# Kernel optimization log

Measured on AMD Instinct MI355X. Metric: run time of the kernel, lower is better.

The kernel has to match this reference:

```python
import jax, jax.numpy as jnp
import numpy as np

B, C, H, W = 64, 3, 64, 64
F = 96          # base_filters
K = 8           # n_mixtures
h, w = H // 2, W // 2
C0 = 2 * C      # channels of each checkerboard half
SECTIONS = [C0, C0, C0 * K, C0 * K, C0 * K]
SPLITS = [int(s) for s in np.cumsum(SECTIONS)[:-1]]
EPS = 1e-6


def conv2d(x, wgt, b):
    y = jax.lax.conv_general_dilated(x, wgt, (1, 1), 'SAME',
                                     dimension_numbers=('NCHW', 'OIHW', 'NCHW'))
    return y + b[None, :, None, None]


def layer_norm(x, g, b, eps=1e-5):
    # nn.LayerNorm(mid_shape): normalize over (C,H,W) per sample
    mu = jnp.mean(x, axis=(1, 2, 3), keepdims=True)
    var = jnp.var(x, axis=(1, 2, 3), keepdims=True)
    return (x - mu) / jnp.sqrt(var + eps) * g[None] + b[None]


def checker_split(z, odd=False):
    Bz, Cz, Hz, Wz = z.shape
    z = z.reshape(Bz, Cz, Hz // 2, 2, Wz // 2, 2)
    p00 = z[:, :, :, 0, :, 0]; p01 = z[:, :, :, 0, :, 1]
    p10 = z[:, :, :, 1, :, 0]; p11 = z[:, :, :, 1, :, 1]
    z0 = jnp.concatenate([p00, p11], axis=1)  # even checkerboard
    z1 = jnp.concatenate([p01, p10], axis=1)  # odd checkerboard
    if odd:
        z0, z1 = z1, z0
    return z0, z1


def checker_merge(z0, z1, odd=False):
    if odd:
        z0, z1 = z1, z0
    Cz = z0.shape[1] // 2
    p00, p11 = z0[:, :Cz], z0[:, Cz:]
    p01, p10 = z1[:, :Cz], z1[:, Cz:]
    Bz, _, hz, wz = p00.shape
    zi = jnp.stack([jnp.stack([p00, p01], axis=-1),
                    jnp.stack([p10, p11], axis=-1)], axis=-2)  # (B,C,h,w,2i,2j)
    z = zi.transpose(0, 1, 2, 4, 3, 5).reshape(Bz, Cz, 2 * hz, 2 * wz)
    return z


def gated_attn(x, qkv_w, qkv_b, proj_w, proj_b):
    Bx, Fx, hx, wx = x.shape
    xf = x.reshape(Bx, Fx, hx * wx).transpose(0, 2, 1)  # (B, L, F)
    qkv = xf @ qkv_w.T + qkv_b
    q, k, v = jnp.split(qkv, 3, axis=-1)
    scores = jnp.einsum('bqf,bkf->bqk', q, k) / jnp.sqrt(jnp.float32(Fx))
    attn = jax.nn.softmax(scores, axis=-1)
    o = jnp.einsum('bqk,bkf->bqf', attn, v)
    g = o @ proj_w.T + proj_b
    ga, gb = jnp.split(g, 2, axis=-1)
    out = xf + ga * jax.nn.sigmoid(gb)  # gated residual
    return out.transpose(0, 2, 1).reshape(Bx, Fx, hx, wx)


def conditioner(z1, conv1_w, conv1_b, gconv_w, gconv_b, ln1_g, ln1_b,
                qkv_w, qkv_b, proj_w, proj_b, ln2_g, ln2_b, conv2_w, conv2_b):
    x = conv2d(z1, conv1_w, conv1_b)
    g = conv2d(x, gconv_w, gconv_b)
    ga, gb = jnp.split(g, 2, axis=1)
    x = x + ga * jax.nn.sigmoid(gb)          # GatedConv2d
    x = layer_norm(x, ln1_g, ln1_b)
    x = gated_attn(x, qkv_w, qkv_b, proj_w, proj_b)
    x = layer_norm(x, ln2_g, ln2_b)
    return conv2d(x, conv2_w, conv2_b)


def _forward(z, log_df_dz, conv1_w, conv1_b, gconv_w, gconv_b, ln1_g, ln1_b,
             qkv_w, qkv_b, proj_w, proj_b, ln2_g, ln2_b, conv2_w, conv2_b,
             a_log_scale, a_bias):
    z0, z1 = checker_split(z)
    params = conditioner(z1, conv1_w, conv1_b, gconv_w, gconv_b, ln1_g, ln1_b,
                         qkv_w, qkv_b, proj_w, proj_b, ln2_g, ln2_b, conv2_w, conv2_b)
    a, b, logpi, mu, s = jnp.split(params, SPLITS, axis=1)
    a = jnp.tanh(a) * a_log_scale + a_bias
    Bz = z0.shape[0]
    logpi = jax.nn.log_softmax(logpi.reshape(Bz, K, C0, h, w), axis=1)
    mu = mu.reshape(Bz, K, C0, h, w)
    s = s.reshape(Bz, K, C0, h, w)
    # mixture-of-logistics CDF
    u = (z0[:, None] - mu) * jnp.exp(-s)
    x = jnp.sum(jnp.exp(logpi) * jax.nn.sigmoid(u), axis=1)
    log_pdf = jax.scipy.special.logsumexp(
        logpi - s + jax.nn.log_sigmoid(u) + jax.nn.log_sigmoid(-u), axis=1)
    log_df_dz = log_df_dz + jnp.sum(log_pdf.reshape(Bz, -1), axis=1)
    # logit transform
    x = jnp.clip(x, EPS, 1.0 - EPS)
    z0n = jnp.log(x) - jnp.log1p(-x)
    log_df_dz = log_df_dz + jnp.sum((-jnp.log(x) - jnp.log1p(-x)).reshape(Bz, -1), axis=1)
    # affine rescale
    z0n = z0n * jnp.exp(a) + b
    log_df_dz = log_df_dz + jnp.sum(a.reshape(Bz, -1), axis=1)
    return checker_merge(z0n, z1), log_df_dz


def setup_inputs() -> dict:
    key = jax.random.key(0)
    ks = jax.random.split(key, 10)
    sc = 0.05
    return dict(
        z=jax.random.normal(ks[0], (B, C, H, W), jnp.float32),
        log_df_dz=jnp.zeros((B,), jnp.float32),
        conv1_w=sc * jax.random.normal(ks[1], (F, C0, 3, 3), jnp.float32),
        conv1_b=jnp.zeros((F,), jnp.float32),
        gconv_w=sc * jax.random.normal(ks[2], (2 * F, F, 3, 3), jnp.float32),
        gconv_b=jnp.zeros((2 * F,), jnp.float32),
        ln1_g=jnp.ones((F, h, w), jnp.float32),
        ln1_b=jnp.zeros((F, h, w), jnp.float32),
        qkv_w=sc * jax.random.normal(ks[3], (3 * F, F), jnp.float32),
        qkv_b=jnp.zeros((3 * F,), jnp.float32),
        proj_w=sc * jax.random.normal(ks[4], (2 * F, F), jnp.float32),
        proj_b=jnp.zeros((2 * F,), jnp.float32),
        ln2_g=jnp.ones((F, h, w), jnp.float32),
        ln2_b=jnp.zeros((F, h, w), jnp.float32),
        conv2_w=sc * jax.random.normal(ks[5], (sum(SECTIONS), F, 3, 3), jnp.float32),
        conv2_b=jnp.zeros((sum(SECTIONS),), jnp.float32),
        a_log_scale=0.01 * jax.random.normal(ks[6], (1,), jnp.float32),
        a_bias=0.01 * jax.random.normal(ks[7], (1,), jnp.float32),
    )


def reference(z, log_df_dz, conv1_w, conv1_b, gconv_w, gconv_b, ln1_g, ln1_b,
              qkv_w, qkv_b, proj_w, proj_b, ln2_g, ln2_b, conv2_w, conv2_b,
              a_log_scale, a_bias):
    return _forward(z, log_df_dz, conv1_w, conv1_b, gconv_w, gconv_b, ln1_g, ln1_b,
                    qkv_w, qkv_b, proj_w, proj_b, ln2_g, ln2_b, conv2_w, conv2_b,
                    a_log_scale, a_bias)
```

## Files before the change

kernel.cpp:

```cpp
#include <hip/hip_runtime.h>
#include <cstdint>
#include <cstddef>


typedef unsigned short u16;
typedef __attribute__((ext_vector_type(8))) short short8;
typedef __attribute__((ext_vector_type(4))) float f32x4;
typedef __attribute__((ext_vector_type(4))) unsigned int u32x4;

__device__ __forceinline__ float sigm(float x){ return 1.0f/(1.0f+__expf(-x)); }

__device__ __forceinline__ u16 f2bf(float f){
    unsigned int u = __float_as_uint(f);
    u += 0x7fffu + ((u >> 16) & 1u);
    return (u16)(u >> 16);
}
__device__ __forceinline__ float bf2f(u16 v){
    unsigned int u = ((unsigned int)v) << 16;
    return __uint_as_float(u);
}

__device__ __forceinline__ float ex2(float x){
    float r; asm("v_exp_f32 %0, %1" : "=v"(r) : "v"(x)); return r;
}
__device__ __forceinline__ unsigned cvtpk(float lo, float hi){
    unsigned r; asm("v_cvt_pk_bf16_f32 %0, %1, %2" : "=v"(r) : "v"(lo), "v"(hi)); return r;
}
__device__ __forceinline__ void plswap32(unsigned &a, unsigned &b){
    asm("v_permlane32_swap_b32 %0, %1" : "+v"(a), "+v"(b));
}
__device__ __forceinline__ void plswap16(unsigned &a, unsigned &b){
    asm("v_permlane16_swap_b32 %0, %1" : "+v"(a), "+v"(b));
}

#define SOFTPACK(S, LACC, PA) do { \
    unsigned pk_[4][2]; \
    _Pragma("unroll") \
    for (int t=0;t<4;++t){ \
        float e0 = ex2(S[t][0]); \
        float e1 = ex2(S[t][1]); \
        float e2 = ex2(S[t][2]); \
        float e3 = ex2(S[t][3]); \
        LACC += (e0+e1)+(e2+e3); \
        pk_[t][0] = cvtpk(e0,e1); \
        pk_[t][1] = cvtpk(e2,e3); \
    } \
    _Pragma("unroll") \
    for (int kk=0;kk<2;++kk){ \
        unsigned a0 = pk_[2*kk][0], b0 = pk_[2*kk+1][0]; \
        unsigned a1 = pk_[2*kk][1], b1 = pk_[2*kk+1][1]; \
        plswap32(a0,b0); plswap16(a0,b0); \
        plswap32(a1,b1); plswap16(a1,b1); \
        u32x4 dw_; dw_[0]=a0; dw_[1]=a1; dw_[2]=b0; dw_[3]=b1; \
        PA[kk] = __builtin_bit_cast(short8, dw_); \
    } \
} while(0)

__global__ __launch_bounds__(256) void k_prep(
    const float* __restrict__ z, const float* __restrict__ c1w, const float* __restrict__ c1b,
    const float* __restrict__ gw, const float* __restrict__ c2w,
    const float* __restrict__ qkvw, const float* __restrict__ pw,
    const float* __restrict__ ln1g, const float* __restrict__ ln1b,
    const float* __restrict__ ln2g, const float* __restrict__ ln2b,
    const float* __restrict__ logdf,
    u16* __restrict__ x1b,
    u16* __restrict__ Wg, u16* __restrict__ W2,
    u16* __restrict__ Wqkv, u16* __restrict__ Wproj,
    float* __restrict__ gt1, float* __restrict__ bt1,
    float* __restrict__ gt2, float* __restrict__ bt2,
    float* __restrict__ outlog)
{
    int blk = blockIdx.x;
    int tid = threadIdx.x;
    __shared__ float tin[6][6][34];
    __shared__ __align__(16) u16 Wc[96][72];
    __shared__ __align__(16) u16 imc[128][72];

    if (blk < 512){
        int b  = blk >> 3;
        int pg = blk & 7;
        int r0 = pg*4;
        for (int e = tid; e < 96*72; e += 256){
            int oc = e/72, k = e%72;
            Wc[oc][k] = (k < 54) ? f2bf(c1w[oc*54 + k]) : (u16)0;
        }
        for (int idx = tid; idx < 6*6*34; idx += 256){
            int c = idx/204, rem = idx%204;
            int rr = rem/34, q = rem%34;
            int ii = r0 - 1 + rr, jj = q - 1;
            float v = 0.f;
            if ((unsigned)ii < 32u && (unsigned)jj < 32u){
                if (c < 3) v = z[((b*3+c)*64 + 2*ii)*64 + (2*jj+1)];
                else       v = z[((b*3+(c-3))*64 + (2*ii+1))*64 + 2*jj];
            }
            tin[c][rr][q] = v;
        }
        __syncthreads();
        for (int e = tid; e < 128*72; e += 256){
            int px = e/72, k = e%72;
            float v = 0.f;
            if (k < 54){
                int c = k/9, rr = (k%9)/3, dcc = k%3;
                v = tin[c][(px>>5)+rr][(px&31)+dcc];
            }
            imc[px][k] = f2bf(v);
        }
        __syncthreads();

        int w = tid >> 6, lane = tid & 63;
        int cc = lane & 15, gg = lane >> 4;
        f32x4 acc[2][6];
        #pragma unroll
        for (int u=0;u<2;++u)
            #pragma unroll
            for (int t=0;t<6;++t) acc[u][t] = (f32x4){0.f,0.f,0.f,0.f};

        #pragma unroll
        for (int ks=0; ks<2; ++ks){
            short8 a0 = *reinterpret_cast<const short8*>(&imc[w*32 + cc     ][ks*32 + 8*gg]);
            short8 a1 = *reinterpret_cast<const short8*>(&imc[w*32 + 16 + cc][ks*32 + 8*gg]);
            #pragma unroll
            for (int t=0; t<6; ++t){
                short8 bb = *reinterpret_cast<const short8*>(&Wc[t*16+cc][ks*32 + 8*gg]);
                acc[0][t] = __builtin_amdgcn_mfma_f32_16x16x32_bf16(a0, bb, acc[0][t], 0,0,0);
                acc[1][t] = __builtin_amdgcn_mfma_f32_16x16x32_bf16(a1, bb, acc[1][t], 0,0,0);
            }
        }

        #pragma unroll
        for (int u=0;u<2;++u){
            int p0 = pg*128 + w*32 + u*16 + gg*4;
            #pragma unroll
            for (int t=0;t<6;++t){
                int oc = t*16+cc;
                float bv = c1b[oc];
                #pragma unroll
                for (int r=0;r<4;++r)
                    x1b[((size_t)(b*1024) + p0 + r)*96 + oc] = f2bf(acc[u][t][r] + bv);
            }
        }
    } else if (blk < 1160){
        int idx = (blk-512)*256 + tid;
        int tap = idx / (192*96);
        int rem = idx - tap*192*96;
        int ocp = rem / 96, ic = rem % 96;
        int obk = ocp/96, r = ocp%96, isB = r/48, i = r%48;
        int oc = obk*48 + i + isB*96;
        Wg[idx] = f2bf(gw[(size_t)(oc*96+ic)*9 + tap]);
    } else if (blk < 1700){
        int idx = (blk-1160)*256 + tid;
        int tap = idx / (160*96);
        int rem = idx - tap*160*96;
        int oc = rem / 96, ic = rem % 96;
        W2[idx] = (oc < 156) ? f2bf(c2w[(size_t)(oc*96+ic)*9 + tap]) : (u16)0;
    } else if (blk < 1808){
        int idx = (blk-1700)*256 + tid;
        Wqkv[idx] = f2bf(qkvw[idx]);
    } else if (blk < 1880){
        int idx = (blk-1808)*256 + tid;
        int ocp = idx / 96, ic = idx % 96;
        int obk = ocp/96, r = ocp%96, isB = r/48, i = r%48;
        int oc = obk*48 + i + isB*96;
        Wproj[idx] = f2bf(pw[(size_t)oc*96 + ic]);
    } else if (blk < 2264){
        int idx = (blk-1880)*256 + tid;
        int c = idx >> 10, p = idx & 1023;
        gt1[p*96 + c] = ln1g[idx];
    } else if (blk < 2648){
        int idx = (blk-2264)*256 + tid;
        int c = idx >> 10, p = idx & 1023;
        bt1[p*96 + c] = ln1b[idx];
    } else if (blk < 3032){
        int idx = (blk-2648)*256 + tid;
        int c = idx >> 10, p = idx & 1023;
        gt2[p*96 + c] = ln2g[idx];
    } else if (blk < 3416){
        int idx = (blk-3032)*256 + tid;
        int c = idx >> 10, p = idx & 1023;
        bt2[p*96 + c] = ln2b[idx];
    } else {
        if (tid < 64) outlog[tid] = logdf[tid];
    }
}

__global__ __launch_bounds__(256,4) void k_gconv(const u16* __restrict__ Xpb,
    const u16* __restrict__ Wt, const float* __restrict__ bias,
    u16* __restrict__ outb, float* __restrict__ partials)
{
    int blk  = blockIdx.x;
    int obk  = blk & 1;
    int pblk = (blk >> 1) & 7;
    int b    = blk >> 4;
    int tid  = threadIdx.x;
    int w = tid >> 6, lane = tid & 63;
    int cc = lane & 15, gg = lane >> 4;

    __shared__ __align__(16) u16 Ws[96][104];
    __shared__ float red[8];

    f32x4 acc[2][6];
    #pragma unroll
    for (int u=0;u<2;++u)
        #pragma unroll
        for (int t=0;t<6;++t) acc[u][t] = (f32x4){0.f,0.f,0.f,0.f};

    int base = pblk*128 + w*32;
    int ia = base >> 5;
    const u16* xb = Xpb + (size_t)b*1024*96;
    const u16* wbase = Wt + (size_t)obk*96*96;

    short8 wreg[5];
    #pragma unroll
    for (int i=0;i<5;++i){
        int c = tid + 256*i;
        if (c < 1152){
            int oc=c/12, ico=(c%12)*8;
            wreg[i] = *reinterpret_cast<const short8*>(wbase + oc*96 + ico);
        }
    }

    for (int tap=0; tap<9; ++tap){
        int dr = tap/3 - 1, dc = tap%3 - 1;
        __syncthreads();
        #pragma unroll
        for (int i=0;i<5;++i){
            int c = tid + 256*i;
            if (c < 1152){
                int oc=c/12, ico=(c%12)*8;
                *reinterpret_cast<short8*>(&Ws[oc][ico]) = wreg[i];
            }
        }
        if (tap < 8){
            const u16* wn = wbase + (size_t)(tap+1)*192*96;
            #pragma unroll
            for (int i=0;i<5;++i){
                int c = tid + 256*i;
                if (c < 1152){
                    int oc=c/12, ico=(c%12)*8;
                    wreg[i] = *reinterpret_cast<const short8*>(wn + oc*96 + ico);
                }
            }
        }
        __syncthreads();

        int ii = ia + dr;
        int jj0 = cc + dc, jj1 = cc + 16 + dc;
        bool rv = ((unsigned)ii < 32u);
        bool v0 = rv && ((unsigned)jj0 < 32u);
        bool v1 = rv && ((unsigned)jj1 < 32u);
        const u16* ar0 = xb + (ptrdiff_t)(ii*32 + jj0)*96 + 8*gg;
        const u16* ar1 = xb + (ptrdiff_t)(ii*32 + jj1)*96 + 8*gg;

        #pragma unroll
        for (int ks=0; ks<3; ++ks){
            short8 a0 = {0,0,0,0,0,0,0,0};
            short8 a1 = {0,0,0,0,0,0,0,0};
            if (v0) a0 = *reinterpret_cast<const short8*>(ar0 + ks*32);
            if (v1) a1 = *reinterpret_cast<const short8*>(ar1 + ks*32);
            #pragma unroll
            for (int t=0; t<6; ++t){
                short8 bb = *reinterpret_cast<const short8*>(&Ws[t*16+cc][ks*32+8*gg]);
                acc[0][t] = __builtin_amdgcn_mfma_f32_16x16x32_bf16(a0, bb, acc[0][t], 0,0,0);
                acc[1][t] = __builtin_amdgcn_mfma_f32_16x16x32_bf16(a1, bb, acc[1][t], 0,0,0);
            }
        }
    }

    float s = 0.f, ssq = 0.f;
    #pragma unroll
    for (int u=0;u<2;++u){
        int p0 = base + u*16 + gg*4;
        #pragma unroll
        for (int t=0;t<3;++t){
            int ocA = obk*48 + t*16+cc;
            float ba = bias[ocA], bbv = bias[ocA+96];
            #pragma unroll
            for (int r=0;r<4;++r){
                float res = bf2f(Xpb[((size_t)b*1024 + p0+r)*96 + ocA]);
                float va = acc[u][t][r]   + ba;
                float vb = acc[u][t+3][r] + bbv;
                float v = res + va*sigm(vb);
                outb[((size_t)b*1024 + p0+r)*96 + ocA] = f2bf(v);
                s += v; ssq += v*v;
            }
        }
    }
    #pragma unroll
    for (int o=32;o>0;o>>=1){ s += __shfl_down(s,o,64); ssq += __shfl_down(ssq,o,64); }
    if (lane==0){ red[w]=s; red[4+w]=ssq; }
    __syncthreads();
    if (tid==0){
        int slot = b*16 + pblk*2 + obk;
        partials[slot*2+0] = red[0]+red[1]+red[2]+red[3];
        partials[slot*2+1] = red[4]+red[5]+red[6]+red[7];
    }
}

__global__ __launch_bounds__(256) void k_lne(const u16* __restrict__ xb,
    const float* __restrict__ gt, const float* __restrict__ bt,
    const float* __restrict__ partials, u16* __restrict__ out)
{
    int b = blockIdx.x / 48, rem = blockIdx.x % 48;
    float s=0.f, ss=0.f;
    #pragma unroll
    for (int i=0;i<16;++i){ s += partials[(b*16+i)*2]; ss += partials[(b*16+i)*2+1]; }
    float mu = s/98304.f;
    float r = rsqrtf(ss/98304.f - mu*mu + 1e-5f);

    int e8 = rem*256 + threadIdx.x;
    size_t base = (size_t)b*98304 + (size_t)e8*8;
    short8 x8 = *reinterpret_cast<const short8*>(xb + base);
    const float* gp = gt + e8*8;
    const float* bp = bt + e8*8;
    short8 o8;
    #pragma unroll
    for (int i=0;i<8;++i)
        o8[i] = (short)f2bf((bf2f((u16)x8[i]) - mu)*r*gp[i] + bp[i]);
    *reinterpret_cast<short8*>(out + base) = o8;
}

__global__ __launch_bounds__(256,4) void k_conv2m(const u16* __restrict__ Xpb,
    const u16* __restrict__ Wt, const float* __restrict__ bias,
    u16* __restrict__ out)
{
    int blk  = blockIdx.x;
    int obk  = blk & 1;
    int pblk = (blk >> 1) & 7;
    int b    = blk >> 4;
    int tid  = threadIdx.x;
    int w = tid >> 6, lane = tid & 63;
    int cc = lane & 15, gg = lane >> 4;

    __shared__ __align__(16) u16 Ws[80][104];

    f32x4 acc[2][5];
    #pragma unroll
    for (int u=0;u<2;++u)
        #pragma unroll
        for (int t=0;t<5;++t) acc[u][t] = (f32x4){0.f,0.f,0.f,0.f};

    int base = pblk*128 + w*32;
    int ia = base >> 5;
    const u16* xb = Xpb + (size_t)b*1024*96;
    const u16* wbase = Wt + (size_t)obk*80*96;

    short8 wreg[4];
    #pragma unroll
    for (int i=0;i<4;++i){
        int c = tid + 256*i;
        if (c < 960){
            int oc=c/12, ico=(c%12)*8;
            wreg[i] = *reinterpret_cast<const short8*>(wbase + oc*96 + ico);
        }
    }

    for (int tap=0; tap<9; ++tap){
        int dr = tap/3 - 1, dc = tap%3 - 1;
        __syncthreads();
        #pragma unroll
        for (int i=0;i<4;++i){
            int c = tid + 256*i;
            if (c < 960){
                int oc=c/12, ico=(c%12)*8;
                *reinterpret_cast<short8*>(&Ws[oc][ico]) = wreg[i];
            }
        }
        if (tap < 8){
            const u16* wn = wbase + (size_t)(tap+1)*160*96;
            #pragma unroll
            for (int i=0;i<4;++i){
                int c = tid + 256*i;
                if (c < 960){
                    int oc=c/12, ico=(c%12)*8;
                    wreg[i] = *reinterpret_cast<const short8*>(wn + oc*96 + ico);
                }
            }
        }
        __syncthreads();

        int ii = ia + dr;
        int jj0 = cc + dc, jj1 = cc + 16 + dc;
        bool rv = ((unsigned)ii < 32u);
        bool v0 = rv && ((unsigned)jj0 < 32u);
        bool v1 = rv && ((unsigned)jj1 < 32u);
        const u16* ar0 = xb + (ptrdiff_t)(ii*32 + jj0)*96 + 8*gg;
        const u16* ar1 = xb + (ptrdiff_t)(ii*32 + jj1)*96 + 8*gg;

        #pragma unroll
        for (int ks=0; ks<3; ++ks){
            short8 a0 = {0,0,0,0,0,0,0,0};
            short8 a1 = {0,0,0,0,0,0,0,0};
            if (v0) a0 = *reinterpret_cast<const short8*>(ar0 + ks*32);
            if (v1) a1 = *reinterpret_cast<const short8*>(ar1 + ks*32);
            #pragma unroll
            for (int t=0; t<5; ++t){
                short8 bb = *reinterpret_cast<const short8*>(&Ws[t*16+cc][ks*32+8*gg]);
                acc[0][t] = __builtin_amdgcn_mfma_f32_16x16x32_bf16(a0, bb, acc[0][t], 0,0,0);
                acc[1][t] = __builtin_amdgcn_mfma_f32_16x16x32_bf16(a1, bb, acc[1][t], 0,0,0);
            }
        }
    }

    #pragma unroll
    for (int u=0;u<2;++u){
        int p0 = base + u*16 + gg*4;
        #pragma unroll
        for (int t=0;t<5;++t){
            int oc = obk*80 + t*16+cc;
            if (oc < 156){
                float bv = bias[oc];
                u16* op = out + ((size_t)b*156 + oc)*1024 + p0;
                #pragma unroll
                for (int r=0;r<4;++r) op[r] = f2bf(acc[u][t][r] + bv);
            }
        }
    }
}

__global__ __launch_bounds__(256,4) void k_qkvm(const u16* __restrict__ Xpb,
    const u16* __restrict__ Wt, const float* __restrict__ bias,
    u16* __restrict__ Qb, u16* __restrict__ Kf, u16* __restrict__ Vf)
{
    int blk  = blockIdx.x;
    int obk  = blk & 1;
    int pblk = (blk >> 1) & 7;
    int b    = blk >> 4;
    int tid  = threadIdx.x;
    int w = tid >> 6, lane = tid & 63;
    int cc = lane & 15, gg = lane >> 4;
    const float scale = 0.14724445f;

    __shared__ __align__(16) u16 Ws[144][104];
    {
        const u16* wp = Wt + (size_t)obk*144*96;
        for (int c = tid; c < 144*12; c += 256){
            int oc = c/12, ico = (c%12)*8;
            *reinterpret_cast<short8*>(&Ws[oc][ico]) =
                *reinterpret_cast<const short8*>(wp + oc*96 + ico);
        }
    }

    f32x4 acc[2][9];
    #pragma unroll
    for (int u=0;u<2;++u)
        #pragma unroll
        for (int t=0;t<9;++t) acc[u][t] = (f32x4){0.f,0.f,0.f,0.f};

    int base = pblk*128 + w*32;
    const u16* xb = Xpb + ((size_t)b*1024 + base)*96;
    __syncthreads();

    #pragma unroll
    for (int ks=0; ks<3; ++ks){
        short8 a0 = *reinterpret_cast<const short8*>(xb + (size_t)cc*96      + ks*32 + 8*gg);
        short8 a1 = *reinterpret_cast<const short8*>(xb + (size_t)(cc+16)*96 + ks*32 + 8*gg);
        #pragma unroll
        for (int t=0; t<9; ++t){
            short8 bb = *reinterpret_cast<const short8*>(&Ws[t*16+cc][ks*32+8*gg]);
            acc[0][t] = __builtin_amdgcn_mfma_f32_16x16x32_bf16(a0, bb, acc[0][t], 0,0,0);
            acc[1][t] = __builtin_amdgcn_mfma_f32_16x16x32_bf16(a1, bb, acc[1][t], 0,0,0);
        }
    }

    #pragma unroll
    for (int u=0;u<2;++u){
        int p0 = base + u*16 + gg*4;
        #pragma unroll
        for (int t=0;t<9;++t){
            int n = obk*144 + t*16+cc;
            float bv = bias[n];
            #pragma unroll
            for (int r=0;r<4;++r){
                int p = p0 + r;
                float av = acc[u][t][r] + bv;
                if (n < 96){
                    Qb[((size_t)(b*1024+p))*96 + n] = f2bf(av*scale);
                } else if (n < 192){
                    int f = n-96;
                    int jt = p>>6, t16 = (p>>4)&3, ccs = p&15;
                    int ks = f>>5, ggs = (f>>3)&3, j = f&7;
                    Kf[(size_t)(b*16+jt)*6144 + (size_t)(((t16*3+ks)*4+ggs)*16+ccs)*8 + j] = f2bf(av);
                } else {
                    int f = n-192;
                    int jt = p>>6, kl = p&63;
                    int kk = kl>>5, ggs = (kl>>3)&3, j = kl&7;
                    int ft = f>>4, ccs = f&15;
                    Vf[(size_t)(b*16+jt)*6144 + (size_t)(((ft*2+kk)*4+ggs)*16+ccs)*8 + j] = f2bf(av);
                }
            }
        }
    }
}

__global__ __launch_bounds__(256,2) void k_attn(const u16* __restrict__ Qb,
    const u16* __restrict__ Kf, const u16* __restrict__ Vf, u16* __restrict__ Ob)
{
    int qt = blockIdx.x >> 6;
    int b  = blockIdx.x & 63;
    int tid = threadIdx.x;
    int w  = tid >> 6;
    int lane = tid & 63;
    int cc = lane & 15;
    int gg = lane >> 4;

    __shared__ __align__(16) u16 Ks[2][6144];
    __shared__ __align__(16) u16 Vs[2][6144];

    int q0 = qt*128 + w*32;

    short8 qf[2][3];
    {
        const u16* qr0 = Qb + ((size_t)(b*1024 + q0 + cc))*96;
        #pragma unroll
        for (int ks=0; ks<3; ++ks){
            qf[0][ks] = *reinterpret_cast<const short8*>(qr0 + ks*32 + 8*gg);
            qf[1][ks] = *reinterpret_cast<const short8*>(qr0 + (size_t)16*96 + ks*32 + 8*gg);
        }
    }

    f32x4 Oacc[2][6];
    #pragma unroll
    for (int u=0;u<2;++u)
        #pragma unroll
        for (int ft=0; ft<6; ++ft) Oacc[u][ft] = (f32x4){0.f,0.f,0.f,0.f};
    float l_acc[2] = {0.f, 0.f};

    const u16* Kb0 = Kf + (size_t)(b*16)*6144;
    const u16* Vb0 = Vf + (size_t)(b*16)*6144;

    short8 kreg[3], vreg[3];
    #pragma unroll
    for (int i=0;i<3;++i){
        int s8 = (tid + 256*i)*8;
        kreg[i] = *reinterpret_cast<const short8*>(Kb0 + s8);
        vreg[i] = *reinterpret_cast<const short8*>(Vb0 + s8);
    }
    #pragma unroll
    for (int i=0;i<3;++i){
        int s8 = (tid + 256*i)*8;
        *reinterpret_cast<short8*>(Ks[0] + s8) = kreg[i];
        *reinterpret_cast<short8*>(Vs[0] + s8) = vreg[i];
    }
    #pragma unroll
    for (int i=0;i<3;++i){
        int s8 = (tid + 256*i)*8;
        kreg[i] = *reinterpret_cast<const short8*>(Kb0 + 6144 + s8);
        vreg[i] = *reinterpret_cast<const short8*>(Vb0 + 6144 + s8);
    }

    for (int jt=0; jt<16; ++jt){
        __syncthreads();
        if (jt < 15){
            int nb = (jt+1)&1;
            #pragma unroll
            for (int i=0;i<3;++i){
                int s8 = (tid + 256*i)*8;
                *reinterpret_cast<short8*>(Ks[nb] + s8) = kreg[i];
                *reinterpret_cast<short8*>(Vs[nb] + s8) = vreg[i];
            }
        }
        if (jt < 14){
            const u16* kn = Kb0 + (size_t)(jt+2)*6144;
            const u16* vn = Vb0 + (size_t)(jt+2)*6144;
            #pragma unroll
            for (int i=0;i<3;++i){
                int s8 = (tid + 256*i)*8;
                kreg[i] = *reinterpret_cast<const short8*>(kn + s8);
                vreg[i] = *reinterpret_cast<const short8*>(vn + s8);
            }
        }

        const u16* Kc = Ks[jt&1];
        const u16* Vc = Vs[jt&1];

        f32x4 S0[4], S1[4];
        #pragma unroll
        for (int t=0;t<4;++t){ S0[t] = (f32x4){0.f,0.f,0.f,0.f}; S1[t] = (f32x4){0.f,0.f,0.f,0.f}; }

        __builtin_amdgcn_s_setprio(1);
        #pragma unroll
        for (int ks=0; ks<3; ++ks){
            #pragma unroll
            for (int t=0; t<4; ++t){
                short8 kb = *reinterpret_cast<const short8*>(Kc + ((t*3+ks)*64 + lane)*8);
                S0[t] = __builtin_amdgcn_mfma_f32_16x16x32_bf16(kb, qf[0][ks], S0[t], 0,0,0);
                S1[t] = __builtin_amdgcn_mfma_f32_16x16x32_bf16(kb, qf[1][ks], S1[t], 0,0,0);
            }
        }
        __builtin_amdgcn_s_setprio(0);

        short8 pa0[2], pa1[2];
        SOFTPACK(S0, l_acc[0], pa0);
        SOFTPACK(S1, l_acc[1], pa1);

        __builtin_amdgcn_s_setprio(1);
        #pragma unroll
        for (int kk=0; kk<2; ++kk){
            #pragma unroll
            for (int ft=0; ft<6; ++ft){
                short8 vb = *reinterpret_cast<const short8*>(Vc + ((ft*2+kk)*64 + lane)*8);
                Oacc[0][ft] = __builtin_amdgcn_mfma_f32_16x16x32_bf16(pa0[kk], vb, Oacc[0][ft], 0,0,0);
                Oacc[1][ft] = __builtin_amdgcn_mfma_f32_16x16x32_bf16(pa1[kk], vb, Oacc[1][ft], 0,0,0);
            }
        }
        __builtin_amdgcn_s_setprio(0);
    }

    #pragma unroll
    for (int u=0;u<2;++u){
        float lv = l_acc[u];
        lv += __shfl_xor(lv, 16, 64);
        lv += __shfl_xor(lv, 32, 64);
        float linv[4];
        #pragma unroll
        for (int r=0;r<4;++r) linv[r] = 1.0f / __shfl(lv, 4*gg + r, 64);
        #pragma unroll
        for (int ft=0; ft<6; ++ft)
            #pragma unroll
            for (int r=0; r<4; ++r)
                Ob[((size_t)(b*1024 + q0 + u*16 + 4*gg + r))*96 + ft*16 + cc]
                    = f2bf(Oacc[u][ft][r]*linv[r]);
    }
}

__global__ __launch_bounds__(256,4) void k_projm(const u16* __restrict__ Opb,
    const u16* __restrict__ Wt, const float* __restrict__ bias,
    const u16* __restrict__ xlnb, u16* __restrict__ outb, float* __restrict__ partials)
{
    int blk  = blockIdx.x;
    int obk  = blk & 1;
    int pblk = (blk >> 1) & 7;
    int b    = blk >> 4;
    int tid  = threadIdx.x;
    int w = tid >> 6, lane = tid & 63;
    int cc = lane & 15, gg = lane >> 4;

    __shared__ __align__(16) u16 Ws[96][104];
    __shared__ float red[8];
    {
        const u16* wp = Wt + (size_t)obk*96*96;
        for (int c = tid; c < 96*12; c += 256){
            int oc = c/12, ico = (c%12)*8;
            *reinterpret_cast<short8*>(&Ws[oc][ico]) =
                *reinterpret_cast<const short8*>(wp + oc*96 + ico);
        }
    }

    f32x4 acc[2][6];
    #pragma unroll
    for (int u=0;u<2;++u)
        #pragma unroll
        for (int t=0;t<6;++t) acc[u][t] = (f32x4){0.f,0.f,0.f,0.f};

    int base = pblk*128 + w*32;
    const u16* xb = Opb + ((size_t)b*1024 + base)*96;
    __syncthreads();

    #pragma unroll
    for (int ks=0; ks<3; ++ks){
        short8 a0 = *reinterpret_cast<const short8*>(xb + (size_t)cc*96      + ks*32 + 8*gg);
        short8 a1 = *reinterpret_cast<const short8*>(xb + (size_t)(cc+16)*96 + ks*32 + 8*gg);
        #pragma unroll
        for (int t=0; t<6; ++t){
            short8 bb = *reinterpret_cast<const short8*>(&Ws[t*16+cc][ks*32+8*gg]);
            acc[0][t] = __builtin_amdgcn_mfma_f32_16x16x32_bf16(a0, bb, acc[0][t], 0,0,0);
            acc[1][t] = __builtin_amdgcn_mfma_f32_16x16x32_bf16(a1, bb, acc[1][t], 0,0,0);
        }
    }

    const u16* resb = xlnb + (size_t)b*1024*96;
    float s = 0.f, ssq = 0.f;
    #pragma unroll
    for (int u=0;u<2;++u){
        int p0 = base + u*16 + gg*4;
        #pragma unroll
        for (int t=0;t<3;++t){
            int ocA = obk*48 + t*16+cc;
            float ba = bias[ocA], bbv = bias[ocA+96];
            #pragma unroll
            for (int r=0;r<4;++r){
                float ga = acc[u][t][r]   + ba;
                float gb = acc[u][t+3][r] + bbv;
                float res = bf2f(resb[(size_t)(p0+r)*96 + ocA]);
                float v = res + ga * sigm(gb);
                outb[((size_t)b*1024 + p0+r)*96 + ocA] = f2bf(v);
                s += v; ssq += v*v;
            }
        }
    }
    #pragma unroll
    for (int o=32;o>0;o>>=1){ s += __shfl_down(s,o,64); ssq += __shfl_down(ssq,o,64); }
    if (lane==0){ red[w]=s; red[4+w]=ssq; }
    __syncthreads();
    if (tid==0){
        int slot = b*16 + pblk*2 + obk;
        partials[slot*2+0] = red[0]+red[1]+red[2]+red[3];
        partials[slot*2+1] = red[4]+red[5]+red[6]+red[7];
    }
}

__global__ __launch_bounds__(256) void k_mix(const float* __restrict__ z,
    const u16* __restrict__ params, const float* __restrict__ a_ls_p,
    const float* __restrict__ a_b_p, float* __restrict__ out_z, float* __restrict__ out_log)
{
    int b = blockIdx.x / 24;
    int rem = blockIdx.x % 24;
    int c0 = rem / 4;
    int pix = (rem & 3)*256 + threadIdx.x;
    int i = pix >> 5, j = pix & 31;
    float als = a_ls_p[0], abv = a_b_p[0];
    const u16* pb = params + (size_t)b*156*1024;
    float logacc = 0.f;

    if (c0 < 3){
        int idx01 = ((b*3+c0)*64 + 2*i)*64 + 2*j+1;
        int idx10 = ((b*3+c0)*64 + 2*i+1)*64 + 2*j;
        out_z[idx01] = z[idx01];
        out_z[idx10] = z[idx10];
    }

    {
        float z0v = (c0<3) ? z[((b*3+c0)*64 + 2*i)*64 + 2*j]
                           : z[((b*3+(c0-3))*64 + 2*i+1)*64 + 2*j+1];
        float a_raw = bf2f(pb[(c0)*1024 + pix]);
        float bco   = bf2f(pb[(6+c0)*1024 + pix]);
        float lp[8], mu[8], sv[8];
        float m1 = -1e30f;
        #pragma unroll
        for (int k=0;k<8;++k){
            lp[k] = bf2f(pb[(12 + k*6 + c0)*1024 + pix]);
            mu[k] = bf2f(pb[(60 + k*6 + c0)*1024 + pix]);
            sv[k] = bf2f(pb[(108 + k*6 + c0)*1024 + pix]);
            m1 = fmaxf(m1, lp[k]);
        }
        float se = 0.f;
        #pragma unroll
        for (int k=0;k<8;++k) se += __expf(lp[k]-m1);
        float lse = m1 + __logf(se);
        float xm = 0.f, mt = -1e30f;
        float t[8];
        #pragma unroll
        for (int k=0;k<8;++k){
            float lpn = lp[k] - lse;
            float u = (z0v - mu[k]) * __expf(-sv[k]);
            float au = fabsf(u);
            xm += __expf(lpn) * (1.f/(1.f+__expf(-u)));
            float lss = -(au + 2.f*log1pf(__expf(-au)));
            float tk = lpn - sv[k] + lss;
            t[k] = tk; mt = fmaxf(mt, tk);
        }
        float se2 = 0.f;
        #pragma unroll
        for (int k=0;k<8;++k) se2 += __expf(t[k]-mt);
        logacc += mt + __logf(se2);
        xm = fminf(fmaxf(xm, 1e-6f), 1.f-1e-6f);
        float lx = __logf(xm), l1x = log1pf(-xm);
        logacc += -lx - l1x;
        float aa = tanhf(a_raw)*als + abv;
        float z0n = (lx - l1x)*__expf(aa) + bco;
        logacc += aa;
        int oidx = (c0<3) ? ((b*3+c0)*64 + 2*i)*64 + 2*j
                          : ((b*3+(c0-3))*64 + 2*i+1)*64 + 2*j+1;
        out_z[oidx] = z0n;
    }

    #pragma unroll
    for (int o=32;o>0;o>>=1) logacc += __shfl_down(logacc, o, 64);
    __shared__ float part[4];
    if ((threadIdx.x&63)==0) part[threadIdx.x>>6] = logacc;
    __syncthreads();
    if (threadIdx.x==0){
        atomicAdd(out_log + b, part[0]+part[1]+part[2]+part[3]);
    }
}

extern "C" void kernel_launch(void* const* d_in, const int* in_sizes, int n_in,
                              void* d_out, int out_size, void* d_ws, size_t ws_size,
                              hipStream_t stream)
{
    const float* z     = (const float*)d_in[0];
    const float* logdf = (const float*)d_in[1];
    const float* c1w   = (const float*)d_in[2];
    const float* c1b   = (const float*)d_in[3];
    const float* gw    = (const float*)d_in[4];
    const float* gcb   = (const float*)d_in[5];
    const float* ln1g  = (const float*)d_in[6];
    const float* ln1b  = (const float*)d_in[7];
    const float* qkvw  = (const float*)d_in[8];
    const float* qkvb  = (const float*)d_in[9];
    const float* pw    = (const float*)d_in[10];
    const float* pbb   = (const float*)d_in[11];
    const float* ln2g  = (const float*)d_in[12];
    const float* ln2b  = (const float*)d_in[13];
    const float* c2w   = (const float*)d_in[14];
    const float* c2b   = (const float*)d_in[15];
    const float* als   = (const float*)d_in[16];
    const float* ab    = (const float*)d_in[17];

    float* out_z   = (float*)d_out;
    float* out_log = out_z + 786432;

    float* ws     = (float*)d_ws;
    u16*   x1b    = (u16*)(ws + 0);
    u16*   xg_b   = (u16*)(ws + 3145728);
    u16*   xlnb   = (u16*)(ws + 6291456);
    u16*   Vf     = (u16*)(ws + 9437184);
    u16*   Ob     = (u16*)(ws + 12582912);
    u16*   x2b    = (u16*)(ws + 15728640);
    u16*   Qb     = x1b;
    u16*   Kf     = xg_b;
    u16*   xln2b  = xlnb;
    u16*   params = (u16*)(ws + 9437184);
    const size_t T = 19660800;
    float* gt1    = ws + T;
    float* bt1    = ws + T + 98304;
    float* gt2    = ws + T + 196608;
    float* bt2    = ws + T + 294912;
    float* part1  = ws + T + 393216;
    float* part2  = ws + T + 395264;
    u16*   Wg     = (u16*)(ws + T + 397568);
    u16*   W2     = (u16*)(ws + T + 480512);
    u16*   Wqkv   = (u16*)(ws + T + 549632);
    u16*   Wproj  = (u16*)(ws + T + 563456);

    k_prep   <<<3417, 256, 0, stream>>>(z, c1w, c1b, gw, c2w, qkvw, pw,
                                        ln1g, ln1b, ln2g, ln2b, logdf,
                                        x1b, Wg, W2, Wqkv, Wproj,
                                        gt1, bt1, gt2, bt2, out_log);
    k_gconv  <<<1024, 256, 0, stream>>>(x1b, Wg, gcb, xg_b, part1);
    k_lne    <<<3072, 256, 0, stream>>>(xg_b, gt1, bt1, part1, xlnb);
    k_qkvm   <<<1024, 256, 0, stream>>>(xlnb, Wqkv, qkvb, Qb, Kf, Vf);
    k_attn   <<<512, 256, 0, stream>>>(Qb, Kf, Vf, Ob);
    k_projm  <<<1024, 256, 0, stream>>>(Ob, Wproj, pbb, xlnb, x2b, part2);
    k_lne    <<<3072, 256, 0, stream>>>(x2b, gt2, bt2, part2, xln2b);
    k_conv2m <<<1024, 256, 0, stream>>>(xln2b, W2, c2b, params);
    k_mix    <<<1536, 256, 0, stream>>>(z, params, als, ab, out_z, out_log);
}
```

Before: 270.5 us.

## Fuse first LayerNorm into QKV and proj GEMMs; DMA pre-swizzled weights to LDS

The first LayerNorm kernel is dropped. Its normalization is now applied on the fly when loading A fragments in the QKV GEMM and again in the proj residual epilogue, so one full activation write and read pass goes away. Weight matrices are reordered in the prep kernel into MFMA fragment order, which lets conv, QKV, proj and attention K/V tiles be copied straight into LDS with global_load_lds. That replaces the register-staged copies and adds double buffering in the conv kernels. In exchange, the LN math is recomputed per fragment and the gamma/beta fp32 tables are read twice, and the workspace buffers are reassigned.

```diff
diff --git a/kernel.cpp b/kernel.cpp
--- a/kernel.cpp
+++ b/kernel.cpp
@@ -18,6 +18,13 @@
 __device__ __forceinline__ float bf2f(u16 v){
     unsigned int u = ((unsigned int)v) << 16;
     return __uint_as_float(u);
+}
+
+__device__ __forceinline__ void dma16(const u16* g, u16* l){
+    __builtin_amdgcn_global_load_lds(
+        (const __attribute__((address_space(1))) void*)g,
+        (__attribute__((address_space(3))) void*)l,
+        16, 0, 0);
 }
 
 __device__ __forceinline__ float ex2(float x){
@@ -56,6 +63,22 @@
     } \
 } while(0)
 
+__device__ __forceinline__ short8 ln_frag(const u16* __restrict__ xg,
+    const float* __restrict__ gt, const float* __restrict__ bt,
+    int p, int c0, float mu, float rr)
+{
+    short8 x8 = *reinterpret_cast<const short8*>(xg + (size_t)p*96 + c0);
+    const float* gp = gt + (size_t)p*96 + c0;
+    const float* bp = bt + (size_t)p*96 + c0;
+    short8 o;
+    #pragma unroll
+    for (int j=0;j<8;++j){
+        float ag = rr*gp[j];
+        o[j] = (short)f2bf(bf2f((u16)x8[j])*ag + (bp[j] - mu*ag));
+    }
+    return o;
+}
+
 __global__ __launch_bounds__(256) void k_prep(
     const float* __restrict__ z, const float* __restrict__ c1w, const float* __restrict__ c1b,
     const float* __restrict__ gw, const float* __restrict__ c2w,
@@ -141,26 +164,57 @@
         }
     } else if (blk < 1160){
         int idx = (blk-512)*256 + tid;
-        int tap = idx / (192*96);
-        int rem = idx - tap*192*96;
-        int ocp = rem / 96, ic = rem % 96;
-        int obk = ocp/96, r = ocp%96, isB = r/48, i = r%48;
-        int oc = obk*48 + i + isB*96;
+        int j = idx & 7;
+        int lane = (idx >> 3) & 63;
+        int fo = idx >> 9;
+        int frag = fo % 18;
+        int tob = fo / 18;
+        int obk = tob & 1, tap = tob >> 1;
+        int t = frag/3, ks = frag%3;
+        int cc = lane & 15, gg = lane >> 4;
+        int ocp = obk*96 + t*16 + cc;
+        int r2 = ocp%96, isB = r2/48, i2 = r2%48;
+        int oc = (ocp/96)*48 + i2 + isB*96;
+        int ic = ks*32 + 8*gg + j;
         Wg[idx] = f2bf(gw[(size_t)(oc*96+ic)*9 + tap]);
     } else if (blk < 1700){
         int idx = (blk-1160)*256 + tid;
-        int tap = idx / (160*96);
-        int rem = idx - tap*160*96;
-        int oc = rem / 96, ic = rem % 96;
+        int j = idx & 7;
+        int lane = (idx >> 3) & 63;
+        int fo = idx >> 9;
+        int frag = fo % 15;
+        int tob = fo / 15;
+        int obk = tob & 1, tap = tob >> 1;
+        int t = frag/3, ks = frag%3;
+        int cc = lane & 15, gg = lane >> 4;
+        int oc = obk*80 + t*16 + cc;
+        int ic = ks*32 + 8*gg + j;
         W2[idx] = (oc < 156) ? f2bf(c2w[(size_t)(oc*96+ic)*9 + tap]) : (u16)0;
     } else if (blk < 1808){
         int idx = (blk-1700)*256 + tid;
-        Wqkv[idx] = f2bf(qkvw[idx]);
+        int j = idx & 7;
+        int lane = (idx >> 3) & 63;
+        int fo = idx >> 9;
+        int frag = fo % 27;
+        int obk = fo / 27;
+        int t = frag/3, ks = frag%3;
+        int cc = lane & 15, gg = lane >> 4;
+        int n = obk*144 + t*16 + cc;
+        int ic = ks*32 + 8*gg + j;
+        Wqkv[idx] = f2bf(qkvw[(size_t)n*96 + ic]);
     } else if (blk < 1880){
         int idx = (blk-1808)*256 + tid;
-        int ocp = idx / 96, ic = idx % 96;
-        int obk = ocp/96, r = ocp%96, isB = r/48, i = r%48;
-        int oc = obk*48 + i + isB*96;
+        int j = idx & 7;
+        int lane = (idx >> 3) & 63;
+        int fo = idx >> 9;
+        int frag = fo % 18;
+        int obk = fo / 18;
+        int t = frag/3, ks = frag%3;
+        int cc = lane & 15, gg = lane >> 4;
+        int ocp = obk*96 + t*16 + cc;
+        int r2 = ocp%96, isB = r2/48, i2 = r2%48;
+        int oc = obk*48 + i2 + isB*96;
+        int ic = ks*32 + 8*gg + j;
         Wproj[idx] = f2bf(pw[(size_t)oc*96 + ic]);
     } else if (blk < 2264){
         int idx = (blk-1880)*256 + tid;
@@ -195,7 +249,7 @@
     int w = tid >> 6, lane = tid & 63;
     int cc = lane & 15, gg = lane >> 4;
 
-    __shared__ __align__(16) u16 Ws[96][104];
+    __shared__ __align__(16) u16 Ws[2][9216];
     __shared__ float red[8];
 
     f32x4 acc[2][6];
@@ -207,41 +261,29 @@
     int base = pblk*128 + w*32;
     int ia = base >> 5;
     const u16* xb = Xpb + (size_t)b*1024*96;
-    const u16* wbase = Wt + (size_t)obk*96*96;
-
-    short8 wreg[5];
-    #pragma unroll
-    for (int i=0;i<5;++i){
-        int c = tid + 256*i;
-        if (c < 1152){
-            int oc=c/12, ico=(c%12)*8;
-            wreg[i] = *reinterpret_cast<const short8*>(wbase + oc*96 + ico);
-        }
-    }
-
-    for (int tap=0; tap<9; ++tap){
-        int dr = tap/3 - 1, dc = tap%3 - 1;
-        __syncthreads();
+
+    {
+        const u16* src = Wt + (size_t)obk*9216;
         #pragma unroll
         for (int i=0;i<5;++i){
             int c = tid + 256*i;
-            if (c < 1152){
-                int oc=c/12, ico=(c%12)*8;
-                *reinterpret_cast<short8*>(&Ws[oc][ico]) = wreg[i];
-            }
-        }
+            if (c < 1152) dma16(src + (size_t)c*8, Ws[0] + (size_t)(w*64+256*i)*8);
+        }
+    }
+
+    for (int tap=0; tap<9; ++tap){
+        __syncthreads();
         if (tap < 8){
-            const u16* wn = wbase + (size_t)(tap+1)*192*96;
+            const u16* src = Wt + (size_t)((tap+1)*2 + obk)*9216;
+            int nb = (tap+1)&1;
             #pragma unroll
             for (int i=0;i<5;++i){
                 int c = tid + 256*i;
-                if (c < 1152){
-                    int oc=c/12, ico=(c%12)*8;
-                    wreg[i] = *reinterpret_cast<const short8*>(wn + oc*96 + ico);
-                }
-            }
-        }
-        __syncthreads();
+                if (c < 1152) dma16(src + (size_t)c*8, Ws[nb] + (size_t)(w*64+256*i)*8);
+            }
+        }
+        const u16* Wc = Ws[tap&1];
+        int dr = tap/3 - 1, dc = tap%3 - 1;
 
         int ii = ia + dr;
         int jj0 = cc + dc, jj1 = cc + 16 + dc;
@@ -259,7 +301,7 @@
             if (v1) a1 = *reinterpret_cast<const short8*>(ar1 + ks*32);
             #pragma unroll
             for (int t=0; t<6; ++t){
-                short8 bb = *reinterpret_cast<const short8*>(&Ws[t*16+cc][ks*32+8*gg]);
+                short8 bb = *reinterpret_cast<const short8*>(Wc + ((size_t)(t*3+ks)*64 + lane)*8);
                 acc[0][t] = __builtin_amdgcn_mfma_f32_16x16x32_bf16(a0, bb, acc[0][t], 0,0,0);
                 acc[1][t] = __builtin_amdgcn_mfma_f32_16x16x32_bf16(a1, bb, acc[1][t], 0,0,0);
             }
@@ -331,7 +373,7 @@
     int w = tid >> 6, lane = tid & 63;
     int cc = lane & 15, gg = lane >> 4;
 
-    __shared__ __align__(16) u16 Ws[80][104];
+    __shared__ __align__(16) u16 Ws[2][7680];
 
     f32x4 acc[2][5];
     #pragma unroll
@@ -342,41 +384,29 @@
     int base = pblk*128 + w*32;
     int ia = base >> 5;
     const u16* xb = Xpb + (size_t)b*1024*96;
-    const u16* wbase = Wt + (size_t)obk*80*96;
-
-    short8 wreg[4];
-    #pragma unroll
-    for (int i=0;i<4;++i){
-        int c = tid + 256*i;
-        if (c < 960){
-            int oc=c/12, ico=(c%12)*8;
-            wreg[i] = *reinterpret_cast<const short8*>(wbase + oc*96 + ico);
-        }
-    }
-
-    for (int tap=0; tap<9; ++tap){
-        int dr = tap/3 - 1, dc = tap%3 - 1;
-        __syncthreads();
+
+    {
+        const u16* src = Wt + (size_t)obk*7680;
         #pragma unroll
         for (int i=0;i<4;++i){
             int c = tid + 256*i;
-            if (c < 960){
-                int oc=c/12, ico=(c%12)*8;
-                *reinterpret_cast<short8*>(&Ws[oc][ico]) = wreg[i];
-            }
-        }
+            if (c < 960) dma16(src + (size_t)c*8, Ws[0] + (size_t)(w*64+256*i)*8);
+        }
+    }
+
+    for (int tap=0; tap<9; ++tap){
+        __syncthreads();
         if (tap < 8){
-            const u16* wn = wbase + (size_t)(tap+1)*160*96;
+            const u16* src = Wt + (size_t)((tap+1)*2 + obk)*7680;
+            int nb = (tap+1)&1;
             #pragma unroll
             for (int i=0;i<4;++i){
                 int c = tid + 256*i;
-                if (c < 960){
-                    int oc=c/12, ico=(c%12)*8;
-                    wreg[i] = *reinterpret_cast<const short8*>(wn + oc*96 + ico);
-                }
-            }
-        }
-        __syncthreads();
+                if (c < 960) dma16(src + (size_t)c*8, Ws[nb] + (size_t)(w*64+256*i)*8);
+            }
+        }
+        const u16* Wc = Ws[tap&1];
+        int dr = tap/3 - 1, dc = tap%3 - 1;
 
         int ii = ia + dr;
         int jj0 = cc + dc, jj1 = cc + 16 + dc;
@@ -394,7 +424,7 @@
             if (v1) a1 = *reinterpret_cast<const short8*>(ar1 + ks*32);
             #pragma unroll
             for (int t=0; t<5; ++t){
-                short8 bb = *reinterpret_cast<const short8*>(&Ws[t*16+cc][ks*32+8*gg]);
+                short8 bb = *reinterpret_cast<const short8*>(Wc + ((size_t)(t*3+ks)*64 + lane)*8);
                 acc[0][t] = __builtin_amdgcn_mfma_f32_16x16x32_bf16(a0, bb, acc[0][t], 0,0,0);
                 acc[1][t] = __builtin_amdgcn_mfma_f32_16x16x32_bf16(a1, bb, acc[1][t], 0,0,0);
             }
@@ -417,7 +447,9 @@
     }
 }
 
-__global__ __launch_bounds__(256,4) void k_qkvm(const u16* __restrict__ Xpb,
+__global__ __launch_bounds__(256,4) void k_qkvm(const u16* __restrict__ Xg,
+    const float* __restrict__ gt, const float* __restrict__ bt,
+    const float* __restrict__ part,
     const u16* __restrict__ Wt, const float* __restrict__ bias,
     u16* __restrict__ Qb, u16* __restrict__ Kf, u16* __restrict__ Vf)
 {
@@ -430,15 +462,21 @@
     int cc = lane & 15, gg = lane >> 4;
     const float scale = 0.14724445f;
 
-    __shared__ __align__(16) u16 Ws[144][104];
+    __shared__ __align__(16) u16 Ws[13824];
     {
-        const u16* wp = Wt + (size_t)obk*144*96;
-        for (int c = tid; c < 144*12; c += 256){
-            int oc = c/12, ico = (c%12)*8;
-            *reinterpret_cast<short8*>(&Ws[oc][ico]) =
-                *reinterpret_cast<const short8*>(wp + oc*96 + ico);
-        }
-    }
+        const u16* src = Wt + (size_t)obk*13824;
+        #pragma unroll
+        for (int i=0;i<7;++i){
+            int c = tid + 256*i;
+            if (c < 1728) dma16(src + (size_t)c*8, Ws + (size_t)(w*64+256*i)*8);
+        }
+    }
+
+    float sS=0.f, sQ=0.f;
+    #pragma unroll
+    for (int i=0;i<16;++i){ sS += part[(b*16+i)*2]; sQ += part[(b*16+i)*2+1]; }
+    float mu = sS/98304.f;
+    float rr = rsqrtf(sQ/98304.f - mu*mu + 1e-5f);
 
     f32x4 acc[2][9];
     #pragma unroll
@@ -447,16 +485,17 @@
         for (int t=0;t<9;++t) acc[u][t] = (f32x4){0.f,0.f,0.f,0.f};
 
     int base = pblk*128 + w*32;
-    const u16* xb = Xpb + ((size_t)b*1024 + base)*96;
+    const u16* xg = Xg + (size_t)b*1024*96;
     __syncthreads();
 
     #pragma unroll
     for (int ks=0; ks<3; ++ks){
-        short8 a0 = *reinterpret_cast<const short8*>(xb + (size_t)cc*96      + ks*32 + 8*gg);
-        short8 a1 = *reinterpret_cast<const short8*>(xb + (size_t)(cc+16)*96 + ks*32 + 8*gg);
+        int c0 = ks*32 + 8*gg;
+        short8 a0 = ln_frag(xg, gt, bt, base+cc,    c0, mu, rr);
+        short8 a1 = ln_frag(xg, gt, bt, base+cc+16, c0, mu, rr);
         #pragma unroll
         for (int t=0; t<9; ++t){
-            short8 bb = *reinterpret_cast<const short8*>(&Ws[t*16+cc][ks*32+8*gg]);
+            short8 bb = *reinterpret_cast<const short8*>(Ws + ((size_t)(t*3+ks)*64 + lane)*8);
             acc[0][t] = __builtin_amdgcn_mfma_f32_16x16x32_bf16(a0, bb, acc[0][t], 0,0,0);
             acc[1][t] = __builtin_amdgcn_mfma_f32_16x16x32_bf16(a1, bb, acc[1][t], 0,0,0);
         }
@@ -528,45 +567,26 @@
     const u16* Kb0 = Kf + (size_t)(b*16)*6144;
     const u16* Vb0 = Vf + (size_t)(b*16)*6144;
 
-    short8 kreg[3], vreg[3];
     #pragma unroll
     for (int i=0;i<3;++i){
-        int s8 = (tid + 256*i)*8;
-        kreg[i] = *reinterpret_cast<const short8*>(Kb0 + s8);
-        vreg[i] = *reinterpret_cast<const short8*>(Vb0 + s8);
-    }
-    #pragma unroll
-    for (int i=0;i<3;++i){
-        int s8 = (tid + 256*i)*8;
-        *reinterpret_cast<short8*>(Ks[0] + s8) = kreg[i];
-        *reinterpret_cast<short8*>(Vs[0] + s8) = vreg[i];
-    }
-    #pragma unroll
-    for (int i=0;i<3;++i){
-        int s8 = (tid + 256*i)*8;
-        kreg[i] = *reinterpret_cast<const short8*>(Kb0 + 6144 + s8);
-        vreg[i] = *reinterpret_cast<const short8*>(Vb0 + 6144 + s8);
+        size_t c8 = (size_t)(tid + 256*i)*8;
+        size_t l8 = (size_t)(w*64 + 256*i)*8;
+        dma16(Kb0 + c8, Ks[0] + l8);
+        dma16(Vb0 + c8, Vs[0] + l8);
     }
 
     for (int jt=0; jt<16; ++jt){
         __syncthreads();
         if (jt < 15){
+            const u16* kn = Kb0 + (size_t)(jt+1)*6144;
+            const u16* vn = Vb0 + (size_t)(jt+1)*6144;
             int nb = (jt+1)&1;
             #pragma unroll
             for (int i=0;i<3;++i){
-                int s8 = (tid + 256*i)*8;
-                *reinterpret_cast<short8*>(Ks[nb] + s8) = kreg[i];
-                *reinterpret_cast<short8*>(Vs[nb] + s8) = vreg[i];
-            }
-        }
-        if (jt < 14){
-            const u16* kn = Kb0 + (size_t)(jt+2)*6144;
-            const u16* vn = Vb0 + (size_t)(jt+2)*6144;
-            #pragma unroll
-            for (int i=0;i<3;++i){
-                int s8 = (tid + 256*i)*8;
-                kreg[i] = *reinterpret_cast<const short8*>(kn + s8);
-                vreg[i] = *reinterpret_cast<const short8*>(vn + s8);
+                size_t c8 = (size_t)(tid + 256*i)*8;
+                size_t l8 = (size_t)(w*64 + 256*i)*8;
+                dma16(kn + c8, Ks[nb] + l8);
+                dma16(vn + c8, Vs[nb] + l8);
             }
         }
 
@@ -625,7 +645,9 @@
 
 __global__ __launch_bounds__(256,4) void k_projm(const u16* __restrict__ Opb,
     const u16* __restrict__ Wt, const float* __restrict__ bias,
-    const u16* __restrict__ xlnb, u16* __restrict__ outb, float* __restrict__ partials)
+    const u16* __restrict__ Xg, const float* __restrict__ gt, const float* __restrict__ bt,
+    const float* __restrict__ part1,
+    u16* __restrict__ outb, float* __restrict__ partials)
 {
     int blk  = blockIdx.x;
     int obk  = blk & 1;
@@ -635,16 +657,22 @@
     int w = tid >> 6, lane = tid & 63;
     int cc = lane & 15, gg = lane >> 4;
 
-    __shared__ __align__(16) u16 Ws[96][104];
+    __shared__ __align__(16) u16 Ws[9216];
     __shared__ float red[8];
     {
-        const u16* wp = Wt + (size_t)obk*96*96;
-        for (int c = tid; c < 96*12; c += 256){
-            int oc = c/12, ico = (c%12)*8;
-            *reinterpret_cast<short8*>(&Ws[oc][ico]) =
-                *reinterpret_cast<const short8*>(wp + oc*96 + ico);
-        }
-    }
+        const u16* src = Wt + (size_t)obk*9216;
+        #pragma unroll
+        for (int i=0;i<5;++i){
+            int c = tid + 256*i;
+            if (c < 1152) dma16(src + (size_t)c*8, Ws + (size_t)(w*64+256*i)*8);
+        }
+    }
+
+    float sS=0.f, sQ=0.f;
+    #pragma unroll
+    for (int i=0;i<16;++i){ sS += part1[(b*16+i)*2]; sQ += part1[(b*16+i)*2+1]; }
+    float mu1 = sS/98304.f;
+    float rr1 = rsqrtf(sQ/98304.f - mu1*mu1 + 1e-5f);
 
     f32x4 acc[2][6];
     #pragma unroll
@@ -662,13 +690,13 @@
         short8 a1 = *reinterpret_cast<const short8*>(xb + (size_t)(cc+16)*96 + ks*32 + 8*gg);
         #pragma unroll
         for (int t=0; t<6; ++t){
-            short8 bb = *reinterpret_cast<const short8*>(&Ws[t*16+cc][ks*32+8*gg]);
+            short8 bb = *reinterpret_cast<const short8*>(Ws + ((size_t)(t*3+ks)*64 + lane)*8);
             acc[0][t] = __builtin_amdgcn_mfma_f32_16x16x32_bf16(a0, bb, acc[0][t], 0,0,0);
             acc[1][t] = __builtin_amdgcn_mfma_f32_16x16x32_bf16(a1, bb, acc[1][t], 0,0,0);
         }
     }
 
-    const u16* resb = xlnb + (size_t)b*1024*96;
+    const u16* resb = Xg + (size_t)b*1024*96;
     float s = 0.f, ssq = 0.f;
     #pragma unroll
     for (int u=0;u<2;++u){
@@ -679,11 +707,13 @@
             float ba = bias[ocA], bbv = bias[ocA+96];
             #pragma unroll
             for (int r=0;r<4;++r){
+                int pl = p0 + r;
                 float ga = acc[u][t][r]   + ba;
                 float gb = acc[u][t+3][r] + bbv;
-                float res = bf2f(resb[(size_t)(p0+r)*96 + ocA]);
+                float xv = bf2f(resb[(size_t)pl*96 + ocA]);
+                float res = (xv - mu1)*rr1*gt[(size_t)pl*96 + ocA] + bt[(size_t)pl*96 + ocA];
                 float v = res + ga * sigm(gb);
-                outb[((size_t)b*1024 + p0+r)*96 + ocA] = f2bf(v);
+                outb[((size_t)b*1024 + pl)*96 + ocA] = f2bf(v);
                 s += v; ssq += v*v;
             }
         }
@@ -803,13 +833,12 @@
     float* ws     = (float*)d_ws;
     u16*   x1b    = (u16*)(ws + 0);
     u16*   xg_b   = (u16*)(ws + 3145728);
-    u16*   xlnb   = (u16*)(ws + 6291456);
+    u16*   Kf     = (u16*)(ws + 6291456);
     u16*   Vf     = (u16*)(ws + 9437184);
     u16*   Ob     = (u16*)(ws + 12582912);
     u16*   x2b    = (u16*)(ws + 15728640);
     u16*   Qb     = x1b;
-    u16*   Kf     = xg_b;
-    u16*   xln2b  = xlnb;
+    u16*   xln2b  = Kf;
     u16*   params = (u16*)(ws + 9437184);
     const size_t T = 19660800;
     float* gt1    = ws + T;
@@ -828,10 +857,9 @@
                                         x1b, Wg, W2, Wqkv, Wproj,
                                         gt1, bt1, gt2, bt2, out_log);
     k_gconv  <<<1024, 256, 0, stream>>>(x1b, Wg, gcb, xg_b, part1);
-    k_lne    <<<3072, 256, 0, stream>>>(xg_b, gt1, bt1, part1, xlnb);
-    k_qkvm   <<<1024, 256, 0, stream>>>(xlnb, Wqkv, qkvb, Qb, Kf, Vf);
+    k_qkvm   <<<1024, 256, 0, stream>>>(xg_b, gt1, bt1, part1, Wqkv, qkvb, Qb, Kf, Vf);
     k_attn   <<<512, 256, 0, stream>>>(Qb, Kf, Vf, Ob);
-    k_projm  <<<1024, 256, 0, stream>>>(Ob, Wproj, pbb, xlnb, x2b, part2);
+    k_projm  <<<1024, 256, 0, stream>>>(Ob, Wproj, pbb, xg_b, gt1, bt1, part1, x2b, part2);
     k_lne    <<<3072, 256, 0, stream>>>(x2b, gt2, bt2, part2, xln2b);
     k_conv2m <<<1024, 256, 0, stream>>>(xln2b, W2, c2b, params);
     k_mix    <<<1536, 256, 0, stream>>>(z, params, als, ab, out_z, out_log);
```

New measurement: 268.6 us. About the same (-0.7%).
